# Optimization experiments

Measured on AMD Instinct MI355X. Metric: run time of the kernel, lower is better.

## Reference

```python
import jax, jax.numpy as jnp
import numpy as np

B, T, H = 64, 1024, 1024


def setup_inputs() -> dict:
    key = jax.random.key(0)
    ks = jax.random.split(key, 8)
    s = 1.0 / np.sqrt(H)
    return {
        "spatial_feats": jax.random.normal(ks[0], (B, T, H), dtype=jnp.float32),
        "hidden_state": jax.random.normal(ks[1], (B, H), dtype=jnp.float32),
        "W_enc": jax.random.uniform(ks[2], (H, H), jnp.float32, -s, s),
        "b_enc": jax.random.uniform(ks[3], (H,), jnp.float32, -s, s),
        "W_dec": jax.random.uniform(ks[4], (H, H), jnp.float32, -s, s),
        "b_dec": jax.random.uniform(ks[5], (H,), jnp.float32, -s, s),
        "w_score": jax.random.uniform(ks[6], (H,), jnp.float32, -s, s),
        "b_score": jax.random.uniform(ks[7], (), jnp.float32, -s, s),
    }


def reference(spatial_feats, hidden_state, W_enc, b_enc, W_dec, b_dec, w_score, b_score):
    # decoder_proj(hidden_state): [B, H] -> [B, 1, H]
    dec = (jnp.einsum("bh,oh->bo", hidden_state, W_dec) + b_dec)[:, None, :]
    # encoder_proj(spatial_feats): [B, T, H]
    enc = jnp.einsum("bth,oh->bto", spatial_feats, W_enc) + b_enc
    energy = jnp.tanh(enc + dec)                      # [B, T, H]
    scores = jnp.einsum("bth,h->bt", energy, w_score) + b_score  # [B, T]
    weights = jax.nn.softmax(scores, axis=1)          # [B, T]
    context = jnp.einsum("bth,bt->bh", spatial_feats, weights)   # [B, H]
    return (context, weights)
```

## Files before the change

kernel.cpp:

```cpp
#include <hip/hip_runtime.h>
#include <hip/hip_bf16.h>
#include <math.h>


typedef __attribute__((ext_vector_type(8))) short bf16x8;
typedef __attribute__((ext_vector_type(8))) unsigned short ushort8;
typedef __attribute__((ext_vector_type(4))) float f32x4;
typedef __attribute__((ext_vector_type(4))) unsigned int u32x4;

__device__ __forceinline__ unsigned short f2bf(float f) {
  union { float f; unsigned int u; } v; v.f = f;
  unsigned int r = v.u + 0x7FFFu + ((v.u >> 16) & 1u);
  return (unsigned short)(r >> 16);
}

__device__ __forceinline__ unsigned int pk2bf(float lo, float hi) {
  return (unsigned int)f2bf(lo) | ((unsigned int)f2bf(hi) << 16);
}

__device__ __forceinline__ float fast_tanh(float x) {
  float e = __expf(2.0f * x);
  return 1.0f - 2.0f / (e + 1.0f);
}

__global__ __launch_bounds__(256) void prep_kernel(
    const float* __restrict__ spatial, const float* __restrict__ hidden,
    const float* __restrict__ W_enc, const float* __restrict__ b_enc,
    const float* __restrict__ W_dec, const float* __restrict__ b_dec,
    unsigned short* __restrict__ Wbf, unsigned short* __restrict__ Abf,
    float* __restrict__ dec, int nCvt) {
  __shared__ float hs[1024];
  const int bid = blockIdx.x, tid = threadIdx.x;
  if (bid < nCvt) {
    const float* src = W_enc;
    unsigned short* dst = Wbf;
    const size_t base = (size_t)bid * 8192 + tid;
    #pragma unroll 4
    for (int i = 0; i < 32; i++) {
      size_t g4 = base + (size_t)i * 256;
      float4 v = ((const float4*)src)[g4];
      ushort4 o;
      o.x = f2bf(v.x); o.y = f2bf(v.y); o.z = f2bf(v.z); o.w = f2bf(v.w);
      *(ushort4*)(dst + g4 * 4) = o;
    }
    return;
  }
  const int dbid = bid - nCvt;
  const int b = dbid >> 3, o0 = (dbid & 7) * 128;
  const int wave = tid >> 6, lane = tid & 63;
  ((float4*)hs)[tid] = ((const float4*)(hidden + (size_t)b * 1024))[tid];
  __syncthreads();
  for (int it = 0; it < 32; it++) {
    int o = o0 + it * 4 + wave;
    const float4* w4 = (const float4*)(W_dec + (size_t)o * 1024);
    float4 acc; acc.x = acc.y = acc.z = acc.w = 0.f;
    #pragma unroll
    for (int j = 0; j < 4; j++) {
      int i = j * 64 + lane;
      float4 x = ((const float4*)hs)[i], y = w4[i];
      acc.x = fmaf(x.x, y.x, acc.x);
      acc.y = fmaf(x.y, y.y, acc.y);
      acc.z = fmaf(x.z, y.z, acc.z);
      acc.w = fmaf(x.w, y.w, acc.w);
    }
    float v = (acc.x + acc.y) + (acc.z + acc.w);
    #pragma unroll
    for (int off = 1; off < 64; off <<= 1) v += __shfl_xor(v, off);
    if (lane == 0) dec[b * 1024 + o] = v + b_dec[o] + b_enc[o];
  }
}

__global__ __launch_bounds__(512, 2) void enc_score_bf16_kernel(
    const float* __restrict__ A,
    const unsigned short* __restrict__ W,
    const float* __restrict__ dec,
    const float* __restrict__ w_score,
    float* __restrict__ scores_p)
{
  __shared__ unsigned short As[2][256][64];
  __shared__ unsigned short Bs[2][256][64];

  const int bid = blockIdx.x;
  const int swz = (bid & 7) * 128 + (bid >> 3);
  const int nt = swz & 3;
  const int m0 = (swz >> 2) * 256;
  const int n0 = nt * 256;
  const int tid = threadIdx.x;
  const int lane = tid & 63, wave = tid >> 6;
  const int wm = (wave >> 2) * 128;
  const int wn = (wave & 3) * 64;
  const int quad = lane >> 4, colL = lane & 15;

  const int s_row = wave * 16 + (lane >> 3);
  const int a_col = (lane & 7) * 8;
  const int w_slot = ((lane & 7) ^ (lane >> 3)) * 8;
  const float* gA = A + (size_t)m0 * 1024;
  const unsigned short* gB = W + (size_t)n0 * 1024;

  const int xs0 = ((0 * 4 + quad) ^ (colL & 7)) * 8;
  const int xs1 = ((1 * 4 + quad) ^ (colL & 7)) * 8;

  float4 rA0[4], rA1[4];
  u32x4  rB0[2], rB1[2];

  auto issueA = [&](int kt, int h, float4* r) {
    const float* src = gA + (size_t)(h * 128 + s_row) * 1024 + kt * 64 + a_col;
    r[0] = *(const float4*)(src);
    r[1] = *(const float4*)(src + 4);
    r[2] = *(const float4*)(src + 8 * 1024);
    r[3] = *(const float4*)(src + 8 * 1024 + 4);
  };
  auto issueB = [&](int kt, int h, u32x4* r) {
    const unsigned short* src =
        gB + (size_t)(h * 128 + s_row) * 1024 + kt * 64 + a_col;
    r[0] = *(const u32x4*)(src);
    r[1] = *(const u32x4*)(src + 8 * 1024);
  };
  auto writeA = [&](int buf, int h, const float4* r) {
    u32x4 p0, p1;
    p0[0] = pk2bf(r[0].x, r[0].y); p0[1] = pk2bf(r[0].z, r[0].w);
    p0[2] = pk2bf(r[1].x, r[1].y); p0[3] = pk2bf(r[1].z, r[1].w);
    p1[0] = pk2bf(r[2].x, r[2].y); p1[1] = pk2bf(r[2].z, r[2].w);
    p1[2] = pk2bf(r[3].x, r[3].y); p1[3] = pk2bf(r[3].z, r[3].w);
    *(u32x4*)(&As[buf][h * 128 + s_row][w_slot]) = p0;
    *(u32x4*)(&As[buf][h * 128 + s_row + 8][w_slot]) = p1;
  };
  auto writeB = [&](int buf, int h, const u32x4* r) {
    *(u32x4*)(&Bs[buf][h * 128 + s_row][w_slot]) = r[0];
    *(u32x4*)(&Bs[buf][h * 128 + s_row + 8][w_slot]) = r[1];
  };

  f32x4 acc[8][4];
  #pragma unroll
  for (int mi = 0; mi < 8; mi++)
    #pragma unroll
    for (int ni = 0; ni < 4; ni++)
      acc[mi][ni] = (f32x4){0.f, 0.f, 0.f, 0.f};

  issueA(0, 0, rA0); issueB(0, 0, rB0);
  issueA(0, 1, rA1); issueB(0, 1, rB1);
  writeA(0, 0, rA0); writeB(0, 0, rB0);
  writeA(0, 1, rA1); writeB(0, 1, rB1);
  asm volatile("s_waitcnt lgkmcnt(0)" ::: "memory");
  __builtin_amdgcn_s_barrier();

  auto ktile = [&](int kt, int buf) {
    bf16x8 bfr[4][2];
    #pragma unroll
    for (int q = 0; q < 4; q++) {
      bf16x8 af[2][2];
      #pragma unroll
      for (int mj = 0; mj < 2; mj++) {
        const int row = wm + (q * 2 + mj) * 16 + colL;
        af[mj][0] = *(const bf16x8*)&As[buf][row][xs0];
        af[mj][1] = *(const bf16x8*)&As[buf][row][xs1];
      }
      if (q == 0) {
        #pragma unroll
        for (int ni = 0; ni < 4; ni++) {
          const int row = wn + ni * 16 + colL;
          bfr[ni][0] = *(const bf16x8*)&Bs[buf][row][xs0];
          bfr[ni][1] = *(const bf16x8*)&Bs[buf][row][xs1];
        }
      }
      if (kt < 15) {
        if (q == 0) { issueA(kt + 1, 0, rA0); issueB(kt + 1, 0, rB0); }
        if (q == 1) { issueA(kt + 1, 1, rA1); issueB(kt + 1, 1, rB1); }
        if (q == 2) { writeA(buf ^ 1, 0, rA0); writeB(buf ^ 1, 0, rB0); }
        if (q == 3) { writeA(buf ^ 1, 1, rA1); writeB(buf ^ 1, 1, rB1); }
      }
      __builtin_amdgcn_sched_barrier(0);
      __builtin_amdgcn_s_barrier();
      asm volatile("s_waitcnt lgkmcnt(0)" ::: "memory");
      __builtin_amdgcn_sched_barrier(0);
      __builtin_amdgcn_s_setprio(1);
      #pragma unroll
      for (int s = 0; s < 2; s++)
        #pragma unroll
        for (int mj = 0; mj < 2; mj++)
          #pragma unroll
          for (int ni = 0; ni < 4; ni++)
            acc[q * 2 + mj][ni] = __builtin_amdgcn_mfma_f32_16x16x32_bf16(
                af[mj][s], bfr[ni][s], acc[q * 2 + mj][ni], 0, 0, 0);
      __builtin_amdgcn_s_setprio(0);
      __builtin_amdgcn_s_barrier();
    }
  };

  for (int ku = 0; ku < 16; ku += 2) {
    ktile(ku, 0);
    ktile(ku + 1, 1);
  }

  const int b = m0 >> 10;
  float decv[4], wsv[4];
  #pragma unroll
  for (int ni = 0; ni < 4; ni++) {
    int n = n0 + wn + ni * 16 + colL;
    decv[ni] = dec[b * 1024 + n];
    wsv[ni] = w_score[n];
  }
  const int slot = nt * 4 + (wave & 3);
  #pragma unroll
  for (int mi = 0; mi < 8; mi++) {
    float rs[4] = {0.f, 0.f, 0.f, 0.f};
    #pragma unroll
    for (int ni = 0; ni < 4; ni++)
      #pragma unroll
      for (int r = 0; r < 4; r++)
        rs[r] += fast_tanh(acc[mi][ni][r] + decv[ni]) * wsv[ni];
    #pragma unroll
    for (int r = 0; r < 4; r++) {
      float v = rs[r];
      v += __shfl_xor(v, 1);
      v += __shfl_xor(v, 2);
      v += __shfl_xor(v, 4);
      v += __shfl_xor(v, 8);
      if (colL == 0)
        scores_p[slot * 65536 + m0 + wm + mi * 16 + quad * 4 + r] = v;
    }
  }
}

__global__ __launch_bounds__(256) void enc_score_f32_kernel(
    const float* __restrict__ A, const float* __restrict__ W,
    const float* __restrict__ dec, const float* __restrict__ w_score,
    float* __restrict__ scores_p) {
  __shared__ unsigned short As[128][32];
  __shared__ unsigned short Bs[128][32];
  const int bid = blockIdx.x;
  const int n0 = (bid & 7) * 128;
  const int m0 = (bid >> 3) * 128;
  const int tid = threadIdx.x;
  const int lane = tid & 63, wave = tid >> 6;
  const int wm = (wave >> 1) * 64, wn = (wave & 1) * 64;
  const int quad = lane >> 4, colL = lane & 15;
  const int srow = tid >> 3;
  const int scol = (tid & 7) * 4;
  f32x4 acc[4][4];
  #pragma unroll
  for (int mi = 0; mi < 4; mi++)
    #pragma unroll
    for (int ni = 0; ni < 4; ni++)
      acc[mi][ni] = (f32x4){0.f, 0.f, 0.f, 0.f};
  for (int k0 = 0; k0 < 1024; k0 += 32) {
    #pragma unroll
    for (int p = 0; p < 4; p++) {
      int r = p * 32 + srow;
      float4 va = *(const float4*)(A + (size_t)(m0 + r) * 1024 + (k0 + scol));
      float4 vb = *(const float4*)(W + (size_t)(n0 + r) * 1024 + (k0 + scol));
      ushort4 pa, pb;
      pa.x = f2bf(va.x); pa.y = f2bf(va.y); pa.z = f2bf(va.z); pa.w = f2bf(va.w);
      pb.x = f2bf(vb.x); pb.y = f2bf(vb.y); pb.z = f2bf(vb.z); pb.w = f2bf(vb.w);
      *(ushort4*)(&As[r][scol]) = pa;
      *(ushort4*)(&Bs[r][scol]) = pb;
    }
    __syncthreads();
    bf16x8 af[4], bfr[4];
    #pragma unroll
    for (int i = 0; i < 4; i++) {
      af[i]  = *(const bf16x8*)(&As[wm + i * 16 + colL][quad * 8]);
      bfr[i] = *(const bf16x8*)(&Bs[wn + i * 16 + colL][quad * 8]);
    }
    #pragma unroll
    for (int mi = 0; mi < 4; mi++)
      #pragma unroll
      for (int ni = 0; ni < 4; ni++)
        acc[mi][ni] = __builtin_amdgcn_mfma_f32_16x16x32_bf16(
            af[mi], bfr[ni], acc[mi][ni], 0, 0, 0);
    __syncthreads();
  }
  const int b = m0 >> 10;
  float decv[4], wsv[4];
  #pragma unroll
  for (int ni = 0; ni < 4; ni++) {
    int n = n0 + wn + ni * 16 + colL;
    decv[ni] = dec[b * 1024 + n];
    wsv[ni] = w_score[n];
  }
  const int slot = (bid & 7) * 2 + (wave & 1);
  #pragma unroll
  for (int mi = 0; mi < 4; mi++) {
    float rsv[4] = {0.f, 0.f, 0.f, 0.f};
    #pragma unroll
    for (int ni = 0; ni < 4; ni++)
      #pragma unroll
      for (int r = 0; r < 4; r++)
        rsv[r] += fast_tanh(acc[mi][ni][r] + decv[ni]) * wsv[ni];
    #pragma unroll
    for (int r = 0; r < 4; r++) {
      float v = rsv[r];
      v += __shfl_xor(v, 1);
      v += __shfl_xor(v, 2);
      v += __shfl_xor(v, 4);
      v += __shfl_xor(v, 8);
      if (colL == 0)
        scores_p[slot * 65536 + m0 + wm + mi * 16 + quad * 4 + r] = v;
    }
  }
}

__global__ void softmax_kernel(const float* __restrict__ scores_p,
                               float* __restrict__ weights,
                               float* __restrict__ context) {
  __shared__ float red[256];
  int b = blockIdx.x, tid = threadIdx.x;
  float4 z; z.x = z.y = z.z = z.w = 0.f;
  ((float4*)context)[blockIdx.x * 256 + tid] = z;
  float v[4];
  float mx = -1e30f;
  #pragma unroll
  for (int i = 0; i < 4; i++) {
    int m = b * 1024 + tid + i * 256;
    float s = 0.f;
    #pragma unroll
    for (int sl = 0; sl < 16; sl++) s += scores_p[sl * 65536 + m];
    v[i] = s;
    mx = fmaxf(mx, v[i]);
  }
  red[tid] = mx; __syncthreads();
  for (int off = 128; off > 0; off >>= 1) {
    if (tid < off) red[tid] = fmaxf(red[tid], red[tid + off]);
    __syncthreads();
  }
  mx = red[0]; __syncthreads();
  float sum = 0.f;
  #pragma unroll
  for (int i = 0; i < 4; i++) { v[i] = __expf(v[i] - mx); sum += v[i]; }
  red[tid] = sum; __syncthreads();
  for (int off = 128; off > 0; off >>= 1) {
    if (tid < off) red[tid] += red[tid + off];
    __syncthreads();
  }
  float inv = 1.0f / red[0];
  #pragma unroll
  for (int i = 0; i < 4; i++) weights[b * 1024 + tid + i * 256] = v[i] * inv;
}

__global__ void context_f32_kernel(const float* __restrict__ spatial,
                                   const float* __restrict__ weights,
                                   float* __restrict__ context) {
  int b = blockIdx.x >> 3, tq = blockIdx.x & 7;
  int tid = threadIdx.x;
  __shared__ float wl[128];
  if (tid < 128) wl[tid] = weights[b * 1024 + tq * 128 + tid];
  __syncthreads();
  const float4* sp =
      (const float4*)(spatial + ((size_t)(b * 1024 + tq * 128)) * 1024);
  float4 acc; acc.x = acc.y = acc.z = acc.w = 0.f;
  #pragma unroll 4
  for (int t = 0; t < 128; t++) {
    float w = wl[t];
    float4 x = sp[(size_t)t * 256 + tid];
    acc.x = fmaf(w, x.x, acc.x);
    acc.y = fmaf(w, x.y, acc.y);
    acc.z = fmaf(w, x.z, acc.z);
    acc.w = fmaf(w, x.w, acc.w);
  }
  float* c = context + b * 1024 + tid * 4;
  atomicAdd(c + 0, acc.x);
  atomicAdd(c + 1, acc.y);
  atomicAdd(c + 2, acc.z);
  atomicAdd(c + 3, acc.w);
}

extern "C" void kernel_launch(void* const* d_in, const int* in_sizes, int n_in,
                              void* d_out, int out_size, void* d_ws, size_t ws_size,
                              hipStream_t stream) {
  const float* spatial  = (const float*)d_in[0];
  const float* hidden   = (const float*)d_in[1];
  const float* W_enc    = (const float*)d_in[2];
  const float* b_enc    = (const float*)d_in[3];
  const float* W_dec    = (const float*)d_in[4];
  const float* b_dec    = (const float*)d_in[5];
  const float* w_score  = (const float*)d_in[6];

  float* out      = (float*)d_out;
  float* context  = out;
  float* weights  = out + 65536;

  float* scores_p = (float*)d_ws;
  float* dec      = scores_p + 16 * 65536;
  unsigned short* Wbf = (unsigned short*)(dec + 65536);

  const size_t need = 16ull * 65536 * 4 + 65536 * 4 + 2ull * 1024 * 1024;

  if (ws_size >= need) {
    const int nCvt = 32;
    prep_kernel<<<nCvt + 512, 256, 0, stream>>>(
        spatial, hidden, W_enc, b_enc, W_dec, b_dec, Wbf, nullptr, dec, nCvt);
    enc_score_bf16_kernel<<<1024, 512, 0, stream>>>(spatial, Wbf, dec,
                                                    w_score, scores_p);
    softmax_kernel<<<64, 256, 0, stream>>>(scores_p, weights, context);
    context_f32_kernel<<<512, 256, 0, stream>>>(spatial, weights, context);
  } else {
    prep_kernel<<<512, 256, 0, stream>>>(
        spatial, hidden, W_enc, b_enc, W_dec, b_dec, nullptr, nullptr, dec,
        0);
    enc_score_f32_kernel<<<4096, 256, 0, stream>>>(spatial, W_enc, dec,
                                                   w_score, scores_p);
    softmax_kernel<<<64, 256, 0, stream>>>(scores_p, weights, context);
    context_f32_kernel<<<512, 256, 0, stream>>>(spatial, weights, context);
  }
}
```

Baseline: 644.6 us.

## Prefetch A tile two k-steps ahead and use hardware bf16 pack conversion

```diff
diff --git a/kernel.cpp b/kernel.cpp
--- a/kernel.cpp
+++ b/kernel.cpp
@@ -15,7 +15,10 @@
 }
 
 __device__ __forceinline__ unsigned int pk2bf(float lo, float hi) {
-  return (unsigned int)f2bf(lo) | ((unsigned int)f2bf(hi) << 16);
+  float2 t; t.x = lo; t.y = hi;
+  __hip_bfloat162 h = __float22bfloat162_rn(t);
+  union { __hip_bfloat162 h; unsigned int u; } c; c.h = h;
+  return c.u;
 }
 
 __device__ __forceinline__ float fast_tanh(float x) {
@@ -100,34 +103,43 @@
   const int xs0 = ((0 * 4 + quad) ^ (colL & 7)) * 8;
   const int xs1 = ((1 * 4 + quad) ^ (colL & 7)) * 8;
 
-  float4 rA0[4], rA1[4];
-  u32x4  rB0[2], rB1[2];
-
-  auto issueA = [&](int kt, int h, float4* r) {
-    const float* src = gA + (size_t)(h * 128 + s_row) * 1024 + kt * 64 + a_col;
-    r[0] = *(const float4*)(src);
-    r[1] = *(const float4*)(src + 4);
-    r[2] = *(const float4*)(src + 8 * 1024);
-    r[3] = *(const float4*)(src + 8 * 1024 + 4);
+  float4 rA0[8], rA1[8];
+  u32x4  rB[4];
+
+  auto issueA = [&](int kt, float4* r) {
+    const float* s0 = gA + (size_t)s_row * 1024 + kt * 64 + a_col;
+    const float* s1 = gA + (size_t)(128 + s_row) * 1024 + kt * 64 + a_col;
+    r[0] = *(const float4*)(s0);
+    r[1] = *(const float4*)(s0 + 4);
+    r[2] = *(const float4*)(s0 + 8 * 1024);
+    r[3] = *(const float4*)(s0 + 8 * 1024 + 4);
+    r[4] = *(const float4*)(s1);
+    r[5] = *(const float4*)(s1 + 4);
+    r[6] = *(const float4*)(s1 + 8 * 1024);
+    r[7] = *(const float4*)(s1 + 8 * 1024 + 4);
   };
-  auto issueB = [&](int kt, int h, u32x4* r) {
-    const unsigned short* src =
-        gB + (size_t)(h * 128 + s_row) * 1024 + kt * 64 + a_col;
-    r[0] = *(const u32x4*)(src);
-    r[1] = *(const u32x4*)(src + 8 * 1024);
+  auto issueB = [&](int kt, u32x4* r) {
+    const unsigned short* s0 = gB + (size_t)s_row * 1024 + kt * 64 + a_col;
+    const unsigned short* s1 =
+        gB + (size_t)(128 + s_row) * 1024 + kt * 64 + a_col;
+    r[0] = *(const u32x4*)(s0);
+    r[1] = *(const u32x4*)(s0 + 8 * 1024);
+    r[2] = *(const u32x4*)(s1);
+    r[3] = *(const u32x4*)(s1 + 8 * 1024);
   };
   auto writeA = [&](int buf, int h, const float4* r) {
+    const float4* p = r + h * 4;
     u32x4 p0, p1;
-    p0[0] = pk2bf(r[0].x, r[0].y); p0[1] = pk2bf(r[0].z, r[0].w);
-    p0[2] = pk2bf(r[1].x, r[1].y); p0[3] = pk2bf(r[1].z, r[1].w);
-    p1[0] = pk2bf(r[2].x, r[2].y); p1[1] = pk2bf(r[2].z, r[2].w);
-    p1[2] = pk2bf(r[3].x, r[3].y); p1[3] = pk2bf(r[3].z, r[3].w);
+    p0[0] = pk2bf(p[0].x, p[0].y); p0[1] = pk2bf(p[0].z, p[0].w);
+    p0[2] = pk2bf(p[1].x, p[1].y); p0[3] = pk2bf(p[1].z, p[1].w);
+    p1[0] = pk2bf(p[2].x, p[2].y); p1[1] = pk2bf(p[2].z, p[2].w);
+    p1[2] = pk2bf(p[3].x, p[3].y); p1[3] = pk2bf(p[3].z, p[3].w);
     *(u32x4*)(&As[buf][h * 128 + s_row][w_slot]) = p0;
     *(u32x4*)(&As[buf][h * 128 + s_row + 8][w_slot]) = p1;
   };
   auto writeB = [&](int buf, int h, const u32x4* r) {
-    *(u32x4*)(&Bs[buf][h * 128 + s_row][w_slot]) = r[0];
-    *(u32x4*)(&Bs[buf][h * 128 + s_row + 8][w_slot]) = r[1];
+    *(u32x4*)(&Bs[buf][h * 128 + s_row][w_slot]) = r[h * 2 + 0];
+    *(u32x4*)(&Bs[buf][h * 128 + s_row + 8][w_slot]) = r[h * 2 + 1];
   };
 
   f32x4 acc[8][4];
@@ -137,14 +149,16 @@
     for (int ni = 0; ni < 4; ni++)
       acc[mi][ni] = (f32x4){0.f, 0.f, 0.f, 0.f};
 
-  issueA(0, 0, rA0); issueB(0, 0, rB0);
-  issueA(0, 1, rA1); issueB(0, 1, rB1);
-  writeA(0, 0, rA0); writeB(0, 0, rB0);
-  writeA(0, 1, rA1); writeB(0, 1, rB1);
+  issueA(0, rA0); issueB(0, rB);
+  writeA(0, 0, rA0); writeA(0, 1, rA0);
+  writeB(0, 0, rB);  writeB(0, 1, rB);
+  issueA(1, rA1);
   asm volatile("s_waitcnt lgkmcnt(0)" ::: "memory");
   __builtin_amdgcn_s_barrier();
 
   auto ktile = [&](int kt, int buf) {
+    const float4* wsrc = buf ? rA0 : rA1;
+    float4*       isrc = buf ? rA1 : rA0;
     bf16x8 bfr[4][2];
     #pragma unroll
     for (int q = 0; q < 4; q++) {
@@ -163,12 +177,13 @@
           bfr[ni][1] = *(const bf16x8*)&Bs[buf][row][xs1];
         }
       }
-      if (kt < 15) {
-        if (q == 0) { issueA(kt + 1, 0, rA0); issueB(kt + 1, 0, rB0); }
-        if (q == 1) { issueA(kt + 1, 1, rA1); issueB(kt + 1, 1, rB1); }
-        if (q == 2) { writeA(buf ^ 1, 0, rA0); writeB(buf ^ 1, 0, rB0); }
-        if (q == 3) { writeA(buf ^ 1, 1, rA1); writeB(buf ^ 1, 1, rB1); }
+      if (q == 0) {
+        if (kt + 2 < 16) issueA(kt + 2, isrc);
+        if (kt + 1 < 16) { issueB(kt + 1, rB); writeA(buf ^ 1, 0, wsrc); }
       }
+      if (q == 1 && kt + 1 < 16) writeA(buf ^ 1, 1, wsrc);
+      if (q == 2 && kt + 1 < 16) writeB(buf ^ 1, 0, rB);
+      if (q == 3 && kt + 1 < 16) writeB(buf ^ 1, 1, rB);
       __builtin_amdgcn_sched_barrier(0);
       __builtin_amdgcn_s_barrier();
       asm volatile("s_waitcnt lgkmcnt(0)" ::: "memory");
```

After: 1.120 ms. +73.7%, slower.

## Prefetch A tiles two k-steps ahead with deeper register buffering

Applied to the files above, without the earlier changes.

```diff
diff --git a/kernel.cpp b/kernel.cpp
--- a/kernel.cpp
+++ b/kernel.cpp
@@ -15,7 +15,10 @@
 }
 
 __device__ __forceinline__ unsigned int pk2bf(float lo, float hi) {
-  return (unsigned int)f2bf(lo) | ((unsigned int)f2bf(hi) << 16);
+  float2 t; t.x = lo; t.y = hi;
+  __hip_bfloat162 h = __float22bfloat162_rn(t);
+  union { __hip_bfloat162 h; unsigned int u; } c; c.h = h;
+  return c.u;
 }
 
 __device__ __forceinline__ float fast_tanh(float x) {
@@ -70,7 +73,86 @@
   }
 }
 
-__global__ __launch_bounds__(512, 2) void enc_score_bf16_kernel(
+#define ISSUE_A(KT, R)                                                        \
+  { const float* sa0_ = gA + (size_t)s_row * 1024 + (KT) * 64 + a_col;        \
+    R[0] = *(const float4*)(sa0_);                                            \
+    R[1] = *(const float4*)(sa0_ + 4);                                        \
+    R[2] = *(const float4*)(sa0_ + 8 * 1024);                                 \
+    R[3] = *(const float4*)(sa0_ + 8 * 1024 + 4);                             \
+    const float* sa1_ = sa0_ + 128 * 1024;                                    \
+    R[4] = *(const float4*)(sa1_);                                            \
+    R[5] = *(const float4*)(sa1_ + 4);                                        \
+    R[6] = *(const float4*)(sa1_ + 8 * 1024);                                 \
+    R[7] = *(const float4*)(sa1_ + 8 * 1024 + 4); }
+
+#define ISSUE_B(KT)                                                           \
+  { const unsigned short* sb0_ =                                              \
+        gB + (size_t)s_row * 1024 + (KT) * 64 + a_col;                        \
+    rB[0] = *(const u32x4*)(sb0_);                                            \
+    rB[1] = *(const u32x4*)(sb0_ + 8 * 1024);                                 \
+    const unsigned short* sb1_ = sb0_ + 128 * 1024;                           \
+    rB[2] = *(const u32x4*)(sb1_);                                            \
+    rB[3] = *(const u32x4*)(sb1_ + 8 * 1024); }
+
+#define WRITE_A(BUFX, H, R)                                                   \
+  { u32x4 p0_, p1_;                                                           \
+    p0_[0] = pk2bf(R[(H)*4+0].x, R[(H)*4+0].y);                               \
+    p0_[1] = pk2bf(R[(H)*4+0].z, R[(H)*4+0].w);                               \
+    p0_[2] = pk2bf(R[(H)*4+1].x, R[(H)*4+1].y);                               \
+    p0_[3] = pk2bf(R[(H)*4+1].z, R[(H)*4+1].w);                               \
+    p1_[0] = pk2bf(R[(H)*4+2].x, R[(H)*4+2].y);                               \
+    p1_[1] = pk2bf(R[(H)*4+2].z, R[(H)*4+2].w);                               \
+    p1_[2] = pk2bf(R[(H)*4+3].x, R[(H)*4+3].y);                               \
+    p1_[3] = pk2bf(R[(H)*4+3].z, R[(H)*4+3].w);                               \
+    *(u32x4*)(&As[BUFX][(H) * 128 + s_row][w_slot]) = p0_;                    \
+    *(u32x4*)(&As[BUFX][(H) * 128 + s_row + 8][w_slot]) = p1_; }
+
+#define WRITE_B(BUFX, H)                                                      \
+  { *(u32x4*)(&Bs[BUFX][(H) * 128 + s_row][w_slot]) = rB[(H) * 2 + 0];        \
+    *(u32x4*)(&Bs[BUFX][(H) * 128 + s_row + 8][w_slot]) = rB[(H) * 2 + 1]; }
+
+#define KTILE(KT, BUFC, RISS, RWR)                                            \
+  { bf16x8 bfr_[4][2];                                                        \
+    _Pragma("unroll")                                                         \
+    for (int q = 0; q < 4; q++) {                                             \
+      bf16x8 af_[2][2];                                                       \
+      _Pragma("unroll")                                                       \
+      for (int mj = 0; mj < 2; mj++) {                                        \
+        const int row_ = wm + (q * 2 + mj) * 16 + colL;                       \
+        af_[mj][0] = *(const bf16x8*)&As[BUFC][row_][xs0];                    \
+        af_[mj][1] = *(const bf16x8*)&As[BUFC][row_][xs1];                    \
+      }                                                                       \
+      if (q == 0) {                                                           \
+        _Pragma("unroll")                                                     \
+        for (int ni = 0; ni < 4; ni++) {                                      \
+          const int row_ = wn + ni * 16 + colL;                               \
+          bfr_[ni][0] = *(const bf16x8*)&Bs[BUFC][row_][xs0];                 \
+          bfr_[ni][1] = *(const bf16x8*)&Bs[BUFC][row_][xs1];                 \
+        }                                                                     \
+        if ((KT) + 2 < 16) ISSUE_A((KT) + 2, RISS);                           \
+        if ((KT) + 1 < 16) { ISSUE_B((KT) + 1); WRITE_A((BUFC) ^ 1, 0, RWR); }\
+      }                                                                       \
+      if (q == 1 && (KT) + 1 < 16) WRITE_A((BUFC) ^ 1, 1, RWR);               \
+      if (q == 2 && (KT) + 1 < 16) WRITE_B((BUFC) ^ 1, 0);                    \
+      if (q == 3 && (KT) + 1 < 16) WRITE_B((BUFC) ^ 1, 1);                    \
+      __builtin_amdgcn_sched_barrier(0);                                      \
+      __builtin_amdgcn_s_barrier();                                           \
+      asm volatile("s_waitcnt lgkmcnt(0)" ::: "memory");                      \
+      __builtin_amdgcn_sched_barrier(0);                                      \
+      __builtin_amdgcn_s_setprio(1);                                          \
+      _Pragma("unroll")                                                       \
+      for (int s = 0; s < 2; s++)                                             \
+        _Pragma("unroll")                                                     \
+        for (int mj = 0; mj < 2; mj++)                                        \
+          _Pragma("unroll")                                                   \
+          for (int ni = 0; ni < 4; ni++)                                      \
+            acc[q * 2 + mj][ni] = __builtin_amdgcn_mfma_f32_16x16x32_bf16(    \
+                af_[mj][s], bfr_[ni][s], acc[q * 2 + mj][ni], 0, 0, 0);       \
+      __builtin_amdgcn_s_setprio(0);                                          \
+      __builtin_amdgcn_s_barrier();                                           \
+    } }
+
+__global__ __launch_bounds__(512, 1) void enc_score_bf16_kernel(
     const float* __restrict__ A,
     const unsigned short* __restrict__ W,
     const float* __restrict__ dec,
@@ -100,35 +182,8 @@
   const int xs0 = ((0 * 4 + quad) ^ (colL & 7)) * 8;
   const int xs1 = ((1 * 4 + quad) ^ (colL & 7)) * 8;
 
-  float4 rA0[4], rA1[4];
-  u32x4  rB0[2], rB1[2];
-
-  auto issueA = [&](int kt, int h, float4* r) {
-    const float* src = gA + (size_t)(h * 128 + s_row) * 1024 + kt * 64 + a_col;
-    r[0] = *(const float4*)(src);
-    r[1] = *(const float4*)(src + 4);
-    r[2] = *(const float4*)(src + 8 * 1024);
-    r[3] = *(const float4*)(src + 8 * 1024 + 4);
-  };
-  auto issueB = [&](int kt, int h, u32x4* r) {
-    const unsigned short* src =
-        gB + (size_t)(h * 128 + s_row) * 1024 + kt * 64 + a_col;
-    r[0] = *(const u32x4*)(src);
-    r[1] = *(const u32x4*)(src + 8 * 1024);
-  };
-  auto writeA = [&](int buf, int h, const float4* r) {
-    u32x4 p0, p1;
-    p0[0] = pk2bf(r[0].x, r[0].y); p0[1] = pk2bf(r[0].z, r[0].w);
-    p0[2] = pk2bf(r[1].x, r[1].y); p0[3] = pk2bf(r[1].z, r[1].w);
-    p1[0] = pk2bf(r[2].x, r[2].y); p1[1] = pk2bf(r[2].z, r[2].w);
-    p1[2] = pk2bf(r[3].x, r[3].y); p1[3] = pk2bf(r[3].z, r[3].w);
-    *(u32x4*)(&As[buf][h * 128 + s_row][w_slot]) = p0;
-    *(u32x4*)(&As[buf][h * 128 + s_row + 8][w_slot]) = p1;
-  };
-  auto writeB = [&](int buf, int h, const u32x4* r) {
-    *(u32x4*)(&Bs[buf][h * 128 + s_row][w_slot]) = r[0];
-    *(u32x4*)(&Bs[buf][h * 128 + s_row + 8][w_slot]) = r[1];
-  };
+  float4 rA0[8], rA1[8];
+  u32x4  rB[4];
 
   f32x4 acc[8][4];
   #pragma unroll
@@ -137,59 +192,16 @@
     for (int ni = 0; ni < 4; ni++)
       acc[mi][ni] = (f32x4){0.f, 0.f, 0.f, 0.f};
 
-  issueA(0, 0, rA0); issueB(0, 0, rB0);
-  issueA(0, 1, rA1); issueB(0, 1, rB1);
-  writeA(0, 0, rA0); writeB(0, 0, rB0);
-  writeA(0, 1, rA1); writeB(0, 1, rB1);
+  ISSUE_A(0, rA0); ISSUE_B(0);
+  WRITE_A(0, 0, rA0); WRITE_A(0, 1, rA0);
+  WRITE_B(0, 0); WRITE_B(0, 1);
+  ISSUE_A(1, rA1);
   asm volatile("s_waitcnt lgkmcnt(0)" ::: "memory");
   __builtin_amdgcn_s_barrier();
 
-  auto ktile = [&](int kt, int buf) {
-    bf16x8 bfr[4][2];
-    #pragma unroll
-    for (int q = 0; q < 4; q++) {
-      bf16x8 af[2][2];
-      #pragma unroll
-      for (int mj = 0; mj < 2; mj++) {
-        const int row = wm + (q * 2 + mj) * 16 + colL;
-        af[mj][0] = *(const bf16x8*)&As[buf][row][xs0];
-        af[mj][1] = *(const bf16x8*)&As[buf][row][xs1];
-      }
-      if (q == 0) {
-        #pragma unroll
-        for (int ni = 0; ni < 4; ni++) {
-          const int row = wn + ni * 16 + colL;
-          bfr[ni][0] = *(const bf16x8*)&Bs[buf][row][xs0];
-          bfr[ni][1] = *(const bf16x8*)&Bs[buf][row][xs1];
-        }
-      }
-      if (kt < 15) {
-        if (q == 0) { issueA(kt + 1, 0, rA0); issueB(kt + 1, 0, rB0); }
-        if (q == 1) { issueA(kt + 1, 1, rA1); issueB(kt + 1, 1, rB1); }
-        if (q == 2) { writeA(buf ^ 1, 0, rA0); writeB(buf ^ 1, 0, rB0); }
-        if (q == 3) { writeA(buf ^ 1, 1, rA1); writeB(buf ^ 1, 1, rB1); }
-      }
-      __builtin_amdgcn_sched_barrier(0);
-      __builtin_amdgcn_s_barrier();
-      asm volatile("s_waitcnt lgkmcnt(0)" ::: "memory");
-      __builtin_amdgcn_sched_barrier(0);
-      __builtin_amdgcn_s_setprio(1);
-      #pragma unroll
-      for (int s = 0; s < 2; s++)
-        #pragma unroll
-        for (int mj = 0; mj < 2; mj++)
-          #pragma unroll
-          for (int ni = 0; ni < 4; ni++)
-            acc[q * 2 + mj][ni] = __builtin_amdgcn_mfma_f32_16x16x32_bf16(
-                af[mj][s], bfr[ni][s], acc[q * 2 + mj][ni], 0, 0, 0);
-      __builtin_amdgcn_s_setprio(0);
-      __builtin_amdgcn_s_barrier();
-    }
-  };
-
   for (int ku = 0; ku < 16; ku += 2) {
-    ktile(ku, 0);
-    ktile(ku + 1, 1);
+    KTILE(ku, 0, rA0, rA1);
+    KTILE(ku + 1, 1, rA1, rA0);
   }
 
   const int b = m0 >> 10;
@@ -221,6 +233,12 @@
     }
   }
 }
+
+#undef ISSUE_A
+#undef ISSUE_B
+#undef WRITE_A
+#undef WRITE_B
+#undef KTILE
 
 __global__ __launch_bounds__(256) void enc_score_f32_kernel(
     const float* __restrict__ A, const float* __restrict__ W,
```

New measurement: 814.6 us. 26.4% more time.
